# Kernel tuning notes

Measured on AMD Instinct MI355X. Metric: run time of the kernel, lower is better.

## Reference

```python
import jax, jax.numpy as jnp
import numpy as np

NUM_TOKS = 16384
TOK_DIM = 256
B, S = 4, 2048


def setup_inputs() -> dict:
    key = jax.random.key(0)
    k1, k2 = jax.random.split(key)
    h = jax.random.normal(k1, (B, S, TOK_DIM), dtype=jnp.float32)
    w = jax.random.normal(k2, (NUM_TOKS, TOK_DIM), dtype=jnp.float32)
    # module normalizes the codebook rows at init
    w = w / jnp.linalg.norm(w, axis=-1, keepdims=True)
    return {"h": h, "weight": w}


def reference(h, weight):
    # Euclidean distance from each h vector to every codebook row:
    # ||h - w||_2 = sqrt(||h||^2 - 2 h.w + ||w||^2)  (GEMM reformulation of
    # the original broadcast-subtract + norm, same math)
    h2 = jnp.sum(h * h, axis=-1, keepdims=True)          # (B, S, 1)
    w2 = jnp.sum(weight * weight, axis=-1)               # (V,)
    cross = jnp.einsum('bsd,vd->bsv', h, weight)         # (B, S, V)
    sq = jnp.maximum(h2 - 2.0 * cross + w2, 0.0)
    return jnp.sqrt(sq)                                  # (B, S, V) distances (logits semantics)
```

## Files before the change

kernel.cpp:

```cpp
#include <hip/hip_runtime.h>
#include <hip/hip_bf16.h>

static constexpr int M_ = 8192;
static constexpr int N_ = 16384;
static constexpr int K_ = 256;
static constexpr int BM = 128, BN = 128, BK = 64;

typedef __attribute__((ext_vector_type(4))) float f32x4;
typedef __attribute__((ext_vector_type(8))) short bf16x8;

__device__ __forceinline__ ushort f2bf(float f) {
  __hip_bfloat16 b = __float2bfloat16(f);
  return __builtin_bit_cast(ushort, b);
}

__global__ __launch_bounds__(256) void cast_rows_k(
    const float* __restrict__ in, ushort* __restrict__ outb,
    float* __restrict__ sq)
{
  const int row  = blockIdx.x * 4 + (threadIdx.x >> 6);
  const int lane = threadIdx.x & 63;
  const float4 v = reinterpret_cast<const float4*>(in)[(size_t)row * 64 + lane];
  ushort4 o;
  o.x = f2bf(v.x); o.y = f2bf(v.y); o.z = f2bf(v.z); o.w = f2bf(v.w);
  reinterpret_cast<ushort4*>(outb)[(size_t)row * 64 + lane] = o;
  float s = v.x * v.x + v.y * v.y + v.z * v.z + v.w * v.w;
  #pragma unroll
  for (int off = 32; off > 0; off >>= 1) s += __shfl_down(s, off, 64);
  if (lane == 0) sq[row] = s;
}

__global__ __launch_bounds__(256) void dist_gemm_k(
    const ushort* __restrict__ A,
    const ushort* __restrict__ Bm,
    const float* __restrict__ h2,
    const float* __restrict__ w2,
    float* __restrict__ C)
{
  __shared__ ushort As[BM * BK];
  __shared__ ushort Bs[BN * BK];

  const int tid  = threadIdx.x;
  const int lane = tid & 63;
  const int wid  = tid >> 6;

  const int nwg = gridDim.x;
  const int cpx = nwg >> 3;
  const int bid = (blockIdx.x & 7) * cpx + (blockIdx.x >> 3);

  const int nbn  = N_ / BN;
  const int brow = (bid / nbn) * BM;
  const int bcol = (bid % nbn) * BN;

  const int wrow = (wid >> 1) * 64;
  const int wcol = (wid & 1) * 64;

  f32x4 acc[4][4] = {};

  const int q0 = wid * 64 + lane;

  for (int kt = 0; kt < K_ / BK; ++kt) {
    #pragma unroll
    for (int it = 0; it < 4; ++it) {
      const int q  = it * 256 + q0;
      const int r  = q >> 3;
      const int ce = (q & 7) * 8;
      const ushort* srcA = A  + (size_t)(brow + r) * K_ + kt * BK + ce;
      const ushort* srcB = Bm + (size_t)(bcol + r) * K_ + kt * BK + ce;
      ushort* dstA = &As[(it * 4 + wid) * 512];
      ushort* dstB = &Bs[(it * 4 + wid) * 512];
      __builtin_amdgcn_global_load_lds(
          (const __attribute__((address_space(1))) unsigned int*)srcA,
          (__attribute__((address_space(3))) unsigned int*)dstA, 16, 0, 0);
      __builtin_amdgcn_global_load_lds(
          (const __attribute__((address_space(1))) unsigned int*)srcB,
          (__attribute__((address_space(3))) unsigned int*)dstB, 16, 0, 0);
    }
    __syncthreads();

    #pragma unroll
    for (int kk = 0; kk < 2; ++kk) {
      bf16x8 af[4], bfr[4];
      const int kb = kk * 32 + ((lane >> 4) * 8);
      #pragma unroll
      for (int i = 0; i < 4; ++i) {
        const int ar = wrow + i * 16 + (lane & 15);
        af[i]  = *reinterpret_cast<const bf16x8*>(&As[ar * BK + kb]);
        const int br = wcol + i * 16 + (lane & 15);
        bfr[i] = *reinterpret_cast<const bf16x8*>(&Bs[br * BK + kb]);
      }
      #pragma unroll
      for (int i = 0; i < 4; ++i)
        #pragma unroll
        for (int j = 0; j < 4; ++j)
          acc[i][j] = __builtin_amdgcn_mfma_f32_16x16x32_bf16(
              af[i], bfr[j], acc[i][j], 0, 0, 0);
    }
    __syncthreads();
  }

  const int cl   = lane & 15;
  const int row0 = brow + wrow + ((lane >> 4) << 2);
  const int col0 = bcol + wcol;
  float h2v[16];
  #pragma unroll
  for (int i = 0; i < 4; ++i)
    #pragma unroll
    for (int r = 0; r < 4; ++r)
      h2v[i * 4 + r] = h2[row0 + i * 16 + r];

  #pragma unroll
  for (int j = 0; j < 4; ++j) {
    const int col  = col0 + j * 16 + cl;
    const float wc = w2[col];
    #pragma unroll
    for (int i = 0; i < 4; ++i) {
      const int row = row0 + i * 16;
      #pragma unroll
      for (int r = 0; r < 4; ++r) {
        const float v = h2v[i * 4 + r] - 2.0f * acc[i][j][r] + wc;
        C[(size_t)(row + r) * N_ + col] = sqrtf(fmaxf(v, 0.0f));
      }
    }
  }
}

__global__ void naive_dist_k(const float* __restrict__ h,
                             const float* __restrict__ w,
                             float* __restrict__ C)
{
  const size_t idx = (size_t)blockIdx.x * 256 + threadIdx.x;
  const int m = (int)(idx / N_);
  const int n = (int)(idx % N_);
  const float* hr = h + (size_t)m * K_;
  const float* wr = w + (size_t)n * K_;
  float dot = 0.f, hh = 0.f, ww = 0.f;
  for (int k = 0; k < K_; ++k) {
    const float a = hr[k], b = wr[k];
    dot += a * b; hh += a * a; ww += b * b;
  }
  C[idx] = sqrtf(fmaxf(hh - 2.0f * dot + ww, 0.0f));
}

extern "C" void kernel_launch(void* const* d_in, const int* in_sizes, int n_in,
                              void* d_out, int out_size, void* d_ws, size_t ws_size,
                              hipStream_t stream) {
  const float* h = (const float*)d_in[0];
  const float* w = (const float*)d_in[1];
  float* out = (float*)d_out;

  const size_t need = (size_t)M_ * K_ * 2 + (size_t)N_ * K_ * 2
                    + (size_t)M_ * 4 + (size_t)N_ * 4;
  if (ws_size < need) {
    naive_dist_k<<<(int)(((size_t)M_ * N_) / 256), 256, 0, stream>>>(h, w, out);
    return;
  }

  ushort* hb = (ushort*)d_ws;
  ushort* wb = hb + (size_t)M_ * K_;
  float*  s1 = (float*)(wb + (size_t)N_ * K_);
  float*  s2 = s1 + M_;

  cast_rows_k<<<M_ / 4, 256, 0, stream>>>(h, hb, s1);
  cast_rows_k<<<N_ / 4, 256, 0, stream>>>(w, wb, s2);
  dist_gemm_k<<<(M_ / BM) * (N_ / BN), 256, 0, stream>>>(hb, wb, s1, s2, out);
}
```

Measured before the change: 662.0 us.

## Load MFMA fragments directly from global with register double-buffering, drop LDS

Removes the LDS staging and both barriers in the GEMM. Each wave now loads its bf16 A/B fragments straight from global memory into registers, prefetching the next K-slice while issuing MFMAs on the current one. Output stores become nontemporal to avoid polluting cache with the large output. In exchange, each element is fetched from global/L2 by both waves that share it instead of once per block, and the per-lane 16-byte row-strided loads are less coalesced.

```diff
diff --git a/kernel.cpp b/kernel.cpp
--- a/kernel.cpp
+++ b/kernel.cpp
@@ -4,7 +4,7 @@
 static constexpr int M_ = 8192;
 static constexpr int N_ = 16384;
 static constexpr int K_ = 256;
-static constexpr int BM = 128, BN = 128, BK = 64;
+static constexpr int BM = 128, BN = 128;
 
 typedef __attribute__((ext_vector_type(4))) float f32x4;
 typedef __attribute__((ext_vector_type(8))) short bf16x8;
@@ -37,12 +37,8 @@
     const float* __restrict__ w2,
     float* __restrict__ C)
 {
-  __shared__ ushort As[BM * BK];
-  __shared__ ushort Bs[BN * BK];
-
-  const int tid  = threadIdx.x;
-  const int lane = tid & 63;
-  const int wid  = tid >> 6;
+  const int lane = threadIdx.x & 63;
+  const int wid  = threadIdx.x >> 6;
 
   const int nwg = gridDim.x;
   const int cpx = nwg >> 3;
@@ -55,48 +51,40 @@
   const int wrow = (wid >> 1) * 64;
   const int wcol = (wid & 1) * 64;
 
+  const int rl = lane & 15;
+  const int kq = (lane >> 4) * 8;
+  const ushort* Ab = A  + (size_t)(brow + wrow + rl) * K_ + kq;
+  const ushort* Bb = Bm + (size_t)(bcol + wcol + rl) * K_ + kq;
+
   f32x4 acc[4][4] = {};
+  bf16x8 a0[4], b0[4], a1[4], b1[4];
 
-  const int q0 = wid * 64 + lane;
+  #pragma unroll
+  for (int i = 0; i < 4; ++i) {
+    a0[i] = *reinterpret_cast<const bf16x8*>(Ab + (size_t)i * 16 * K_);
+    b0[i] = *reinterpret_cast<const bf16x8*>(Bb + (size_t)i * 16 * K_);
+  }
 
-  for (int kt = 0; kt < K_ / BK; ++kt) {
-    #pragma unroll
-    for (int it = 0; it < 4; ++it) {
-      const int q  = it * 256 + q0;
-      const int r  = q >> 3;
-      const int ce = (q & 7) * 8;
-      const ushort* srcA = A  + (size_t)(brow + r) * K_ + kt * BK + ce;
-      const ushort* srcB = Bm + (size_t)(bcol + r) * K_ + kt * BK + ce;
-      ushort* dstA = &As[(it * 4 + wid) * 512];
-      ushort* dstB = &Bs[(it * 4 + wid) * 512];
-      __builtin_amdgcn_global_load_lds(
-          (const __attribute__((address_space(1))) unsigned int*)srcA,
-          (__attribute__((address_space(3))) unsigned int*)dstA, 16, 0, 0);
-      __builtin_amdgcn_global_load_lds(
-          (const __attribute__((address_space(1))) unsigned int*)srcB,
-          (__attribute__((address_space(3))) unsigned int*)dstB, 16, 0, 0);
-    }
-    __syncthreads();
-
-    #pragma unroll
-    for (int kk = 0; kk < 2; ++kk) {
-      bf16x8 af[4], bfr[4];
-      const int kb = kk * 32 + ((lane >> 4) * 8);
+  #pragma unroll
+  for (int kk = 0; kk < 8; ++kk) {
+    const bf16x8* ac = (kk & 1) ? a1 : a0;
+    const bf16x8* bc = (kk & 1) ? b1 : b0;
+    bf16x8* an = (kk & 1) ? a0 : a1;
+    bf16x8* bn = (kk & 1) ? b0 : b1;
+    if (kk < 7) {
+      const int ko = (kk + 1) * 32;
       #pragma unroll
       for (int i = 0; i < 4; ++i) {
-        const int ar = wrow + i * 16 + (lane & 15);
-        af[i]  = *reinterpret_cast<const bf16x8*>(&As[ar * BK + kb]);
-        const int br = wcol + i * 16 + (lane & 15);
-        bfr[i] = *reinterpret_cast<const bf16x8*>(&Bs[br * BK + kb]);
+        an[i] = *reinterpret_cast<const bf16x8*>(Ab + (size_t)i * 16 * K_ + ko);
+        bn[i] = *reinterpret_cast<const bf16x8*>(Bb + (size_t)i * 16 * K_ + ko);
       }
+    }
+    #pragma unroll
+    for (int i = 0; i < 4; ++i)
       #pragma unroll
-      for (int i = 0; i < 4; ++i)
-        #pragma unroll
-        for (int j = 0; j < 4; ++j)
-          acc[i][j] = __builtin_amdgcn_mfma_f32_16x16x32_bf16(
-              af[i], bfr[j], acc[i][j], 0, 0, 0);
-    }
-    __syncthreads();
+      for (int j = 0; j < 4; ++j)
+        acc[i][j] = __builtin_amdgcn_mfma_f32_16x16x32_bf16(
+            ac[i], bc[j], acc[i][j], 0, 0, 0);
   }
 
   const int cl   = lane & 15;
@@ -119,7 +107,8 @@
       #pragma unroll
       for (int r = 0; r < 4; ++r) {
         const float v = h2v[i * 4 + r] - 2.0f * acc[i][j][r] + wc;
-        C[(size_t)(row + r) * N_ + col] = sqrtf(fmaxf(v, 0.0f));
+        __builtin_nontemporal_store(sqrtf(fmaxf(v, 0.0f)),
+                                    &C[(size_t)(row + r) * N_ + col]);
       }
     }
   }
```

Measured after the change: 715.9 us. 8.1% more time.
